# Kernel tuning notes

Measured on AMD Instinct MI355X. Metric: run time of the kernel, lower is better.

## Reference

```python
import jax, jax.numpy as jnp
import numpy as np

TOP_K = 8
NUM_EXPERTS = 64
TEMPERATURE = 1.0
ALPHA = 0.01
EPS = 1e-20


def setup_inputs() -> dict:
    key = jax.random.key(0)
    k1, k2 = jax.random.split(key)
    hidden_states = jax.random.normal(k1, (4, 8192, 1024), dtype=jnp.float32)
    # kaiming_uniform-ish scale for the router weight
    bound = 1.0 / np.sqrt(1024.0)
    weight = jax.random.uniform(k2, (NUM_EXPERTS, 1024), dtype=jnp.float32,
                                minval=-bound, maxval=bound)
    return {"hidden_states": hidden_states, "weight": weight}


def reference(hidden_states, weight):
    bsz, seq_len, hidden_dim = hidden_states.shape
    flat = hidden_states.reshape(-1, hidden_dim)            # [N, H], N = bsz*seq_len
    logits = jnp.einsum('nh,eh->ne', flat, weight) / TEMPERATURE  # [N, E]
    scores = jax.nn.softmax(logits, axis=-1)                # [N, E]
    topk_weight, topk_idx = jax.lax.top_k(scores, TOP_K)    # [N, k] each
    # renormalize top-k probabilities
    topk_weight = topk_weight / (topk_weight.sum(axis=-1, keepdims=True) + EPS)
    # aux load-balancing loss (seq_aux=False branch), scores detached
    scores_aux = jax.lax.stop_gradient(scores)
    idx_flat = topk_idx.reshape(-1)                         # [N*k]
    ce = jnp.zeros((NUM_EXPERTS,), dtype=jnp.float32).at[idx_flat].add(1.0)
    ce = ce / idx_flat.shape[0]                             # mean of one-hot rows
    pi = scores_aux.mean(axis=0)                            # [E]
    fi = ce * NUM_EXPERTS
    aux_loss = (pi * fi).sum() * ALPHA
    return topk_idx, topk_weight, aux_loss
```

## Files before the change

kernel.cpp:

```cpp
#include <hip/hip_runtime.h>

#define H 1024
#define E 64
#define BT 64
#define THETA 2e-4f

typedef __attribute__((ext_vector_type(4))) float f4;
typedef __attribute__((ext_vector_type(16))) float f32x16;
typedef __bf16 bf16x8 __attribute__((ext_vector_type(8)));
typedef unsigned int u32;
typedef __attribute__((ext_vector_type(4))) u32 u32x4;

__device__ __forceinline__ u32 cvtpk_bf16(float a, float b) {
    u32 r;
    asm("v_cvt_pk_bf16_f32 %0, %1, %2" : "=v"(r) : "v"(a), "v"(b));
    return r;
}
__device__ __forceinline__ float asfloat(u32 u) { union { u32 u; float f; } c; c.u = u; return c.f; }

__device__ __forceinline__ void split8(f4 a, f4 b, u32x4& hi, u32x4& lo) {
    float x0[4] = {a.x, a.z, b.x, b.z};
    float x1[4] = {a.y, a.w, b.y, b.w};
    #pragma unroll
    for (int i = 0; i < 4; ++i) {
        u32 h = cvtpk_bf16(x0[i], x1[i]);
        float r0 = x0[i] - asfloat(h << 16);
        float r1 = x1[i] - asfloat(h & 0xFFFF0000u);
        hi[i] = h;
        lo[i] = cvtpk_bf16(r0, r1);
    }
}

__device__ __forceinline__ void async16(const void* g, void* l) {
    __builtin_amdgcn_global_load_lds(
        (const __attribute__((address_space(1))) unsigned int*)g,
        (__attribute__((address_space(3))) unsigned int*)l,
        16, 0, 0);
}

__global__ __launch_bounds__(512, 4)
void gate_main(const float* __restrict__ hs, const float* __restrict__ wt,
               float* __restrict__ out, float* __restrict__ pi_ws,
               float* __restrict__ ce_ws, unsigned int* __restrict__ risk_cnt,
               unsigned int* __restrict__ risk_list, unsigned int risk_cap,
               int n_tokens) {
    __shared__ float smem[16384];
    const int t = threadIdx.x;
    const int wave = t >> 6, lane = t & 63;
    const int tok_base = blockIdx.x * BT;

    const int lr  = lane & 31;
    const int kh  = lane >> 5;
    const int q4  = wave & 3;
    const int kh2 = wave >> 2;
    const int wrow = (q4 >> 1) * 32;
    const int wcol = (q4 & 1) * 32;

    f32x16 acc0, acc1;
    #pragma unroll
    for (int i = 0; i < 16; ++i) { acc0[i] = 0.f; acc1[i] = 0.f; }

    char* sb = (char*)smem;

    auto stage = [&](int c, int b) {
        char* bb = sb + b * 32768;
        #pragma unroll
        for (int q = 0; q < 4; ++q) {
            const int L = q * 512 + t;
            const int r = (L >> 4) & 63;
            const int j = L & 15;
            const int srcj = j ^ (r & 7);
            const float* src = (q < 2)
                ? hs + (size_t)(tok_base + r) * H + c * 64 + srcj * 4
                : wt + (size_t)r * H + c * 64 + srcj * 4;
            async16(src, bb + ((q * 512 + wave * 64) << 4));
        }
    };

    stage(0, 0);
    const int arow = wrow + lr;
    const int brow = wcol + lr;
    const int abase = arow * 256;
    const int bbase = 16384 + brow * 256;
    const int asw = arow & 7, bsw = brow & 7;

    #pragma unroll 2
    for (int c = 0; c < 16; ++c) {
        __syncthreads();
        if (c < 15) stage(c + 1, (c + 1) & 1);
        const char* cb = sb + (c & 1) * 32768;
        #pragma unroll
        for (int ks = 0; ks < 2; ++ks) {
            const int s = kh2 * 8 + ks * 4 + kh * 2;
            f4 a0 = *(const f4*)(cb + abase + ((s ^ asw) << 4));
            f4 a1 = *(const f4*)(cb + abase + (((s + 1) ^ asw) << 4));
            f4 b0 = *(const f4*)(cb + bbase + ((s ^ bsw) << 4));
            f4 b1 = *(const f4*)(cb + bbase + (((s + 1) ^ bsw) << 4));
            u32x4 ahp, alp, bhp, blp;
            split8(a0, a1, ahp, alp);
            split8(b0, b1, bhp, blp);
            const bf16x8 ah = __builtin_bit_cast(bf16x8, ahp);
            const bf16x8 al = __builtin_bit_cast(bf16x8, alp);
            const bf16x8 bh = __builtin_bit_cast(bf16x8, bhp);
            const bf16x8 bl = __builtin_bit_cast(bf16x8, blp);
            acc0 = __builtin_amdgcn_mfma_f32_32x32x16_bf16(ah, bh, acc0, 0, 0, 0);
            acc1 = __builtin_amdgcn_mfma_f32_32x32x16_bf16(ah, bl, acc1, 0, 0, 0);
            acc1 = __builtin_amdgcn_mfma_f32_32x32x16_bf16(al, bh, acc1, 0, 0, 0);
        }
    }
    __syncthreads();

    float* S = smem;
    f4* S4 = (f4*)smem;
    float* P2    = smem + 4352;
    float* recip = smem + 8448;
    float* hist  = smem + 8512;
    float* pi7   = smem + 8576;

    {
        float vs[16];
        #pragma unroll
        for (int i = 0; i < 16; ++i) vs[i] = acc0[i] + acc1[i];
        if (kh2) {
            #pragma unroll
            for (int gq = 0; gq < 4; ++gq)
                #pragma unroll
                for (int qq = 0; qq < 4; ++qq)
                    P2[q4 * 1024 + (qq + gq * 8 + kh * 4) * 32 + lr] = vs[gq * 4 + qq];
        }
        if (t < 64) hist[t] = 0.f;
        __syncthreads();
        if (!kh2) {
            #pragma unroll
            for (int gq = 0; gq < 4; ++gq)
                #pragma unroll
                for (int qq = 0; qq < 4; ++qq) {
                    const int row = qq + gq * 8 + kh * 4;
                    S[(wrow + row) * 68 + wcol + lr] =
                        vs[gq * 4 + qq] + P2[q4 * 1024 + row * 32 + lr];
                }
        }
    }
    __syncthreads();

    if (t < 256) {
        const int tok = t >> 2, q = t & 3;
        f4 v[4];
        #pragma unroll
        for (int c2 = 0; c2 < 4; ++c2) v[c2] = S4[tok * 17 + q * 4 + c2];
        float m = v[0].x;
        #pragma unroll
        for (int c2 = 0; c2 < 4; ++c2)
            m = fmaxf(m, fmaxf(fmaxf(v[c2].x, v[c2].y), fmaxf(v[c2].z, v[c2].w)));
        m = fmaxf(m, __shfl_xor(m, 1, 64));
        m = fmaxf(m, __shfl_xor(m, 2, 64));
        float lsum = 0.f;
        #pragma unroll
        for (int c2 = 0; c2 < 4; ++c2) {
            v[c2].x = __expf(v[c2].x - m); v[c2].y = __expf(v[c2].y - m);
            v[c2].z = __expf(v[c2].z - m); v[c2].w = __expf(v[c2].w - m);
            lsum += (v[c2].x + v[c2].y) + (v[c2].z + v[c2].w);
        }
        #pragma unroll
        for (int c2 = 0; c2 < 4; ++c2) S4[tok * 17 + q * 4 + c2] = v[c2];
        lsum += __shfl_xor(lsum, 1, 64);
        lsum += __shfl_xor(lsum, 2, 64);
        if (q == 0) recip[tok] = 1.0f / lsum;
    }
    __syncthreads();

    const int selw = blockIdx.x & 7;
    if (wave == selw) {
        const int tok = lane;
        const int tok_g = tok_base + tok;
        float val[9]; int idx[9];
        #pragma unroll
        for (int r = 0; r < 9; ++r) { val[r] = -1.f; idx[r] = 0; }
        #pragma unroll
        for (int c2 = 0; c2 < 16; ++c2) {
            f4 v = S4[tok * 17 + c2];
            float e4[4] = {v.x, v.y, v.z, v.w};
            #pragma unroll
            for (int u = 0; u < 4; ++u) {
                float cv = e4[u]; int ci = c2 * 4 + u;
                #pragma unroll
                for (int r = 0; r < 9; ++r) {
                    const bool g = cv > val[r];
                    const float tv = val[r]; const int ti = idx[r];
                    val[r] = g ? cv : tv;  idx[r] = g ? ci : ti;
                    cv = g ? tv : cv;      ci = g ? ti : ci;
                }
            }
        }
        const float s8 = ((val[0] + val[1]) + (val[2] + val[3]))
                       + ((val[4] + val[5]) + (val[6] + val[7]));
        const float wsum = s8 + 1e-20f;
        f4* out4 = (f4*)out;
        f4 o;
        o.x = (float)idx[0]; o.y = (float)idx[1]; o.z = (float)idx[2]; o.w = (float)idx[3];
        out4[(size_t)tok_g * 2] = o;
        o.x = (float)idx[4]; o.y = (float)idx[5]; o.z = (float)idx[6]; o.w = (float)idx[7];
        out4[(size_t)tok_g * 2 + 1] = o;
        const size_t wb = (size_t)n_tokens * 2;
        o.x = val[0] / wsum; o.y = val[1] / wsum; o.z = val[2] / wsum; o.w = val[3] / wsum;
        out4[wb + (size_t)tok_g * 2] = o;
        o.x = val[4] / wsum; o.y = val[5] / wsum; o.z = val[6] / wsum; o.w = val[7] / wsum;
        out4[wb + (size_t)tok_g * 2 + 1] = o;
        #pragma unroll
        for (int r = 0; r < 8; ++r) atomicAdd(&hist[idx[r]], 1.0f);
        float ming = 1e30f;
        #pragma unroll
        for (int r = 0; r < 8; ++r)
            ming = fminf(ming, (val[r] - val[r + 1]) / fmaxf(val[r], 1e-30f));
        if (ming < THETA) {
            unsigned int pos = atomicAdd(risk_cnt, 1u);
            if (pos < risk_cap) risk_list[pos] = (unsigned int)tok_g;
        }
    } else {
        const int sev = ((wave - selw) & 7) - 1;
        const int e = lane;
        const int t0 = sev * 9;
        const int t1 = (sev == 6) ? 64 : (t0 + 9);
        float part = 0.f;
        for (int tok = t0; tok < t1; ++tok)
            part = fmaf(S[tok * 68 + e], recip[tok], part);
        pi7[sev * 64 + e] = part;
    }
    __syncthreads();
    if (t < 64) {
        const float p = ((pi7[t] + pi7[64 + t]) + (pi7[128 + t] + pi7[192 + t]))
                      + ((pi7[256 + t] + pi7[320 + t]) + pi7[384 + t]);
        atomicAdd(&pi_ws[t], p);
    } else if (t < 128) {
        atomicAdd(&ce_ws[t - 64], hist[t - 64]);
    }
}

__global__ __launch_bounds__(256)
void gate_fixup(const float* __restrict__ hs, const float* __restrict__ wt,
                float* __restrict__ out, const unsigned int* __restrict__ risk_cnt,
                const unsigned int* __restrict__ risk_list, unsigned int risk_cap,
                int n_tokens, const float* __restrict__ pi_ws,
                const float* __restrict__ ce_ws) {
    __shared__ float hrow[H];
    __shared__ double red[256];
    const int t = threadIdx.x;

    if (blockIdx.x == 0 && t < 64) {
        double pi = (double)pi_ws[t] / (double)n_tokens;
        double ce = (double)ce_ws[t] / ((double)n_tokens * 8.0);
        double term = pi * ce * 64.0;
        #pragma unroll
        for (int off = 32; off > 0; off >>= 1) term += __shfl_xor(term, off, 64);
        if (t == 0) out[(size_t)n_tokens * 16] = (float)(term * 0.01);
    }

    unsigned int cnt = *risk_cnt;
    if (cnt > risk_cap) cnt = risk_cap;

    for (unsigned int u = blockIdx.x; u < cnt; u += gridDim.x) {
        const int tok = (int)risk_list[u];
        ((float4*)hrow)[t] = ((const float4*)(hs + (size_t)tok * H))[t];
        __syncthreads();

        const int e = t >> 2, sl = t & 3;
        const float4* wp = (const float4*)wt + (size_t)e * 256;
        const float4* hp = (const float4*)hrow;
        double acc = 0.0;
        #pragma unroll 8
        for (int k4 = 0; k4 < 64; ++k4) {
            float4 wv = wp[k4 * 4 + sl];
            float4 hv = hp[k4 * 4 + sl];
            acc = fma((double)wv.x, (double)hv.x, acc);
            acc = fma((double)wv.y, (double)hv.y, acc);
            acc = fma((double)wv.z, (double)hv.z, acc);
            acc = fma((double)wv.w, (double)hv.w, acc);
        }
        red[t] = acc;
        __syncthreads();

        if (t < 64) {
            const int lane = t;
            double lg = red[t * 4] + red[t * 4 + 1] + red[t * 4 + 2] + red[t * 4 + 3];
            double m = lg;
            #pragma unroll
            for (int off = 32; off > 0; off >>= 1) {
                double o = __shfl_xor(m, off, 64);
                m = (o > m) ? o : m;
            }
            const double p = exp(lg - m);
            double v = lg, psum = 0.0, mypv = 0.0;
            int myidx = 0;
            for (int r = 0; r < 8; ++r) {
                double bv = v; int bi = lane;
                #pragma unroll
                for (int off = 32; off > 0; off >>= 1) {
                    double ov = __shfl_xor(bv, off, 64);
                    int    oi = __shfl_xor(bi, off, 64);
                    if (ov > bv || (ov == bv && oi < bi)) { bv = ov; bi = oi; }
                }
                double pw = __shfl(p, bi, 64);
                psum += pw;
                if (lane == r) { myidx = bi; mypv = pw; }
                if (lane == bi) v = -1e300;
            }
            const double wsum = psum + 1e-20;
            if (lane < 8) {
                out[(size_t)tok * 8 + lane] = (float)myidx;
                out[(size_t)n_tokens * 8 + (size_t)tok * 8 + lane] = (float)(mypv / wsum);
            }
        }
        __syncthreads();
    }
}

extern "C" void kernel_launch(void* const* d_in, const int* in_sizes, int n_in,
                              void* d_out, int out_size, void* d_ws, size_t ws_size,
                              hipStream_t stream) {
    const float* hs = (const float*)d_in[0];
    const float* wt = (const float*)d_in[1];
    float* out = (float*)d_out;
    const int n_tokens = in_sizes[0] / H;

    float* pi_ws = (float*)d_ws;
    float* ce_ws = (float*)((char*)d_ws + 256);
    unsigned int* risk_cnt  = (unsigned int*)((char*)d_ws + 512);
    unsigned int* risk_list = (unsigned int*)((char*)d_ws + 1024);
    unsigned int risk_cap = (unsigned int)((ws_size > 1024 ? (ws_size - 1024) : 0) / 4);
    if (risk_cap > (unsigned int)n_tokens) risk_cap = (unsigned int)n_tokens;

    size_t zbytes = ws_size < 1024 ? ws_size : 1024;
    hipMemsetAsync(d_ws, 0, zbytes, stream);

    gate_main<<<n_tokens / BT, 512, 0, stream>>>(hs, wt, out, pi_ws, ce_ws,
                                                 risk_cnt, risk_list, risk_cap, n_tokens);
    gate_fixup<<<256, 256, 0, stream>>>(hs, wt, out, risk_cnt, risk_list, risk_cap,
                                        n_tokens, pi_ws, ce_ws);
}
```

Baseline: 251.4 us.

## Deepen LDS pipeline to four stages and replicate aux-loss atomic targets

The GEMM main loop now works on 32-wide K chunks through a 4-buffer LDS ring with three chunks prefetched. Each thread issues one A and one B async load per stage, and the loop waits with explicit vmcnt counts plus raw barriers instead of a full __syncthreads per double-buffer step. This is meant to hide global-load latency better. Separately, the per-block pi/ce atomics are spread over 8 replicas keyed by block index to reduce contention, and the fixup kernel sums the replicas. The cost is a larger workspace region to zero and more barrier iterations, each doing less compute.

```diff
diff --git a/kernel.cpp b/kernel.cpp
--- a/kernel.cpp
+++ b/kernel.cpp
@@ -48,66 +48,67 @@
     const int t = threadIdx.x;
     const int wave = t >> 6, lane = t & 63;
     const int tok_base = blockIdx.x * BT;
-
-    const int lr  = lane & 31;
-    const int kh  = lane >> 5;
-    const int q4  = wave & 3;
-    const int kh2 = wave >> 2;
+    char* sb = (char*)smem;
+
+    const int srow = t >> 3;
+    const int srcj = (t & 7) ^ (srow & 7);
+    const float* gA = hs + (size_t)(tok_base + srow) * H + srcj * 4;
+    const float* gB = wt + (size_t)srow * H + srcj * 4;
+    const int sdest = wave << 10;
+
+    const int lr = lane & 31, kh = lane >> 5;
+    const int q4 = wave & 3, kh2 = wave >> 2;
     const int wrow = (q4 >> 1) * 32;
     const int wcol = (q4 & 1) * 32;
+    const int arow = wrow + lr, brow = wcol + lr;
+    const int s0 = kh2 * 4 + kh * 2;
+    const int aoff = arow * 128 + ((s0 ^ (arow & 7)) << 4);
+    const int boff = 8192 + brow * 128 + ((s0 ^ (brow & 7)) << 4);
 
     f32x16 acc0, acc1;
     #pragma unroll
     for (int i = 0; i < 16; ++i) { acc0[i] = 0.f; acc1[i] = 0.f; }
 
-    char* sb = (char*)smem;
-
-    auto stage = [&](int c, int b) {
-        char* bb = sb + b * 32768;
-        #pragma unroll
-        for (int q = 0; q < 4; ++q) {
-            const int L = q * 512 + t;
-            const int r = (L >> 4) & 63;
-            const int j = L & 15;
-            const int srcj = j ^ (r & 7);
-            const float* src = (q < 2)
-                ? hs + (size_t)(tok_base + r) * H + c * 64 + srcj * 4
-                : wt + (size_t)r * H + c * 64 + srcj * 4;
-            async16(src, bb + ((q * 512 + wave * 64) << 4));
-        }
+    auto stage = [&](int c) {
+        char* bb = sb + (c & 3) * 16384;
+        async16(gA + c * 32, bb + sdest);
+        async16(gB + c * 32, bb + 8192 + sdest);
     };
-
-    stage(0, 0);
-    const int arow = wrow + lr;
-    const int brow = wcol + lr;
-    const int abase = arow * 256;
-    const int bbase = 16384 + brow * 256;
-    const int asw = arow & 7, bsw = brow & 7;
-
-    #pragma unroll 2
-    for (int c = 0; c < 16; ++c) {
-        __syncthreads();
-        if (c < 15) stage(c + 1, (c + 1) & 1);
-        const char* cb = sb + (c & 1) * 32768;
-        #pragma unroll
-        for (int ks = 0; ks < 2; ++ks) {
-            const int s = kh2 * 8 + ks * 4 + kh * 2;
-            f4 a0 = *(const f4*)(cb + abase + ((s ^ asw) << 4));
-            f4 a1 = *(const f4*)(cb + abase + (((s + 1) ^ asw) << 4));
-            f4 b0 = *(const f4*)(cb + bbase + ((s ^ bsw) << 4));
-            f4 b1 = *(const f4*)(cb + bbase + (((s + 1) ^ bsw) << 4));
-            u32x4 ahp, alp, bhp, blp;
-            split8(a0, a1, ahp, alp);
-            split8(b0, b1, bhp, blp);
-            const bf16x8 ah = __builtin_bit_cast(bf16x8, ahp);
-            const bf16x8 al = __builtin_bit_cast(bf16x8, alp);
-            const bf16x8 bh = __builtin_bit_cast(bf16x8, bhp);
-            const bf16x8 bl = __builtin_bit_cast(bf16x8, blp);
-            acc0 = __builtin_amdgcn_mfma_f32_32x32x16_bf16(ah, bh, acc0, 0, 0, 0);
-            acc1 = __builtin_amdgcn_mfma_f32_32x32x16_bf16(ah, bl, acc1, 0, 0, 0);
-            acc1 = __builtin_amdgcn_mfma_f32_32x32x16_bf16(al, bh, acc1, 0, 0, 0);
-        }
-    }
+    auto compute = [&](int c) {
+        const char* cb = sb + (c & 3) * 16384;
+        f4 a0 = *(const f4*)(cb + aoff);
+        f4 a1 = *(const f4*)(cb + (aoff ^ 16));
+        f4 b0 = *(const f4*)(cb + boff);
+        f4 b1 = *(const f4*)(cb + (boff ^ 16));
+        u32x4 ahp, alp, bhp, blp;
+        split8(a0, a1, ahp, alp);
+        split8(b0, b1, bhp, blp);
+        const bf16x8 ah = __builtin_bit_cast(bf16x8, ahp);
+        const bf16x8 al = __builtin_bit_cast(bf16x8, alp);
+        const bf16x8 bh = __builtin_bit_cast(bf16x8, bhp);
+        const bf16x8 bl = __builtin_bit_cast(bf16x8, blp);
+        acc0 = __builtin_amdgcn_mfma_f32_32x32x16_bf16(ah, bh, acc0, 0, 0, 0);
+        acc1 = __builtin_amdgcn_mfma_f32_32x32x16_bf16(ah, bl, acc1, 0, 0, 0);
+        acc1 = __builtin_amdgcn_mfma_f32_32x32x16_bf16(al, bh, acc1, 0, 0, 0);
+    };
+
+    stage(0); stage(1); stage(2);
+    for (int c = 0; c < 30; ++c) {
+        asm volatile("s_waitcnt vmcnt(4)" ::: "memory");
+        __builtin_amdgcn_s_barrier();
+        __builtin_amdgcn_sched_barrier(0);
+        if (c < 29) stage(c + 3);
+        __builtin_amdgcn_sched_barrier(0);
+        compute(c);
+    }
+    asm volatile("s_waitcnt vmcnt(2)" ::: "memory");
+    __builtin_amdgcn_s_barrier();
+    __builtin_amdgcn_sched_barrier(0);
+    compute(30);
+    asm volatile("s_waitcnt vmcnt(0)" ::: "memory");
+    __builtin_amdgcn_s_barrier();
+    __builtin_amdgcn_sched_barrier(0);
+    compute(31);
     __syncthreads();
 
     float* S = smem;
@@ -227,12 +228,13 @@
         pi7[sev * 64 + e] = part;
     }
     __syncthreads();
+    const int rep = (blockIdx.x & 7) << 6;
     if (t < 64) {
         const float p = ((pi7[t] + pi7[64 + t]) + (pi7[128 + t] + pi7[192 + t]))
                       + ((pi7[256 + t] + pi7[320 + t]) + pi7[384 + t]);
-        atomicAdd(&pi_ws[t], p);
+        atomicAdd(&pi_ws[rep + t], p);
     } else if (t < 128) {
-        atomicAdd(&ce_ws[t - 64], hist[t - 64]);
+        atomicAdd(&ce_ws[rep + (t - 64)], hist[t - 64]);
     }
 }
 
@@ -247,8 +249,14 @@
     const int t = threadIdx.x;
 
     if (blockIdx.x == 0 && t < 64) {
-        double pi = (double)pi_ws[t] / (double)n_tokens;
-        double ce = (double)ce_ws[t] / ((double)n_tokens * 8.0);
+        double pi = 0.0, ce = 0.0;
+        #pragma unroll
+        for (int rp = 0; rp < 8; ++rp) {
+            pi += (double)pi_ws[rp * 64 + t];
+            ce += (double)ce_ws[rp * 64 + t];
+        }
+        pi /= (double)n_tokens;
+        ce /= ((double)n_tokens * 8.0);
         double term = pi * ce * 64.0;
         #pragma unroll
         for (int off = 32; off > 0; off >>= 1) term += __shfl_xor(term, off, 64);
@@ -323,13 +331,13 @@
     const int n_tokens = in_sizes[0] / H;
 
     float* pi_ws = (float*)d_ws;
-    float* ce_ws = (float*)((char*)d_ws + 256);
-    unsigned int* risk_cnt  = (unsigned int*)((char*)d_ws + 512);
-    unsigned int* risk_list = (unsigned int*)((char*)d_ws + 1024);
-    unsigned int risk_cap = (unsigned int)((ws_size > 1024 ? (ws_size - 1024) : 0) / 4);
+    float* ce_ws = (float*)((char*)d_ws + 2048);
+    unsigned int* risk_cnt  = (unsigned int*)((char*)d_ws + 4096);
+    unsigned int* risk_list = (unsigned int*)((char*)d_ws + 4608);
+    unsigned int risk_cap = (unsigned int)((ws_size > 4608 ? (ws_size - 4608) : 0) / 4);
     if (risk_cap > (unsigned int)n_tokens) risk_cap = (unsigned int)n_tokens;
 
-    size_t zbytes = ws_size < 1024 ? ws_size : 1024;
+    size_t zbytes = ws_size < 4608 ? ws_size : 4608;
     hipMemsetAsync(d_ws, 0, zbytes, stream);
 
     gate_main<<<n_tokens / BT, 512, 0, stream>>>(hs, wt, out, pi_ws, ce_ws,
```

Result: faster. 238.5 us (-5.1%).
